# Kernel tuning notes

Hardware: AMD Instinct MI355X
Metric: run time of the kernel (lower is better)

## Reference

```python
import jax, jax.numpy as jnp
import numpy as np

N_NODES = 100000
N_EDGES = 1600000
N_GRAPHS = 512


def setup_inputs() -> dict:
    key = jax.random.key(0)
    k = jax.random.split(key, 6)
    x = jax.random.normal(k[0], (N_NODES, 768), dtype=jnp.float32)
    edge_index = jax.random.randint(k[1], (2, N_EDGES), 0, N_NODES, dtype=jnp.int32)
    batch = jnp.sort(jax.random.randint(k[2], (N_NODES,), 0, N_GRAPHS, dtype=jnp.int32))
    W1 = jax.random.normal(k[3], (768, 256), dtype=jnp.float32) * 0.02
    b1 = jnp.zeros((256,), dtype=jnp.float32)
    W2 = jax.random.normal(k[4], (256, 2), dtype=jnp.float32) * 0.02
    b2 = jnp.zeros((2,), dtype=jnp.float32)
    return {"x": x, "edge_index": edge_index, "batch": batch,
            "W1": W1, "b1": b1, "W2": W2, "b2": b2}


def gcn_conv(x, src, dst, W, b, n_nodes):
    # PyG GCNConv: h = x @ W; add self-loops; symmetric normalization D^-1/2 A D^-1/2
    h = x @ W  # [N, out]
    ones = jnp.ones((src.shape[0],), dtype=x.dtype)
    # degree including self-loop
    deg = jax.ops.segment_sum(ones, dst, num_segments=n_nodes) + 1.0  # [N]
    dinv = jax.lax.rsqrt(deg)
    norm_e = dinv[src] * dinv[dst]  # [E]
    msg = h[src] * norm_e[:, None]  # gather + scale, [E, out]
    agg = jax.ops.segment_sum(msg, dst, num_segments=n_nodes)  # scatter-add
    # self-loop contribution: norm = dinv[i]*dinv[i] = 1/deg[i]
    agg = agg + h * (1.0 / deg)[:, None]
    return agg + b


def reference(x, edge_index, batch, W1, b1, W2, b2):
    n_nodes = x.shape[0]
    src, dst = edge_index[0], edge_index[1]
    h = gcn_conv(x, src, dst, W1, b1, n_nodes)
    h = jax.nn.relu(h)
    # dropout p=0.5 is identity in eval mode (self.training=False)
    h = gcn_conv(h, src, dst, W2, b2, n_nodes)
    # global_mean_pool over batch assignment
    sums = jax.ops.segment_sum(h, batch, num_segments=N_GRAPHS)  # [G, out]
    counts = jax.ops.segment_sum(jnp.ones((n_nodes,), h.dtype), batch, num_segments=N_GRAPHS)
    return sums / jnp.maximum(counts, 1.0)[:, None]
```

## Files before the change

kernel.cpp:

```cpp
#include <hip/hip_runtime.h>

typedef unsigned short u16;
typedef unsigned int   u32;
typedef __bf16 bf16x8 __attribute__((ext_vector_type(8)));
typedef float  f32x4  __attribute__((ext_vector_type(4)));
typedef u32    u32x4  __attribute__((ext_vector_type(4)));
typedef u16    u16x8  __attribute__((ext_vector_type(8)));

#define NF1 768
#define NF2 256

__device__ __forceinline__ u16 f2bf(float f) {
  u32 u = __builtin_bit_cast(u32, f);
  u += 0x7fffu + ((u >> 16) & 1u);
  return (u16)(u >> 16);
}
__device__ __forceinline__ float bf2f(u16 h) {
  return __builtin_bit_cast(float, ((u32)h) << 16);
}

__device__ __forceinline__ void gll16(const void* g, void* l) {
  __builtin_amdgcn_global_load_lds(
      (const __attribute__((address_space(1))) unsigned int*)g,
      (__attribute__((address_space(3))) unsigned int*)l, 16, 0, 0);
}

__global__ void k_zero(u32* __restrict__ p, int n) {
  int i = blockIdx.x * 256 + threadIdx.x;
  if (i < n) p[i] = 0u;
}

__global__ void k_w1t(const float* __restrict__ W1, u16* __restrict__ W1T) {
  int idx = blockIdx.x * 256 + threadIdx.x;
  if (idx < NF1 * NF2) {
    int k = idx >> 8, j = idx & 255;
    W1T[(size_t)j * NF1 + k] = f2bf(W1[idx]);
  }
}

__global__ __launch_bounds__(256) void k_gemm(const float* __restrict__ X,
                                              const u16* __restrict__ W1T,
                                              u16* __restrict__ H1, int M) {
  __shared__ float lsA[128 * 64];
  __shared__ u16   lsB[128 * 64];
  const int t    = threadIdx.x;
  const int m0   = blockIdx.x * 128;
  const int n0   = blockIdx.y * 128;
  const int lane = t & 63;
  const int wid  = t >> 6;
  const int wr   = wid >> 1, wc = wid & 1;

  const int rowbase = wid * 4 + (lane >> 4);
  const int perm_s  = ((rowbase & 7) << 1) | ((rowbase >> 3) & 1);
  const float* srcA[8];
  #pragma unroll
  for (int i = 0; i < 8; ++i) {
    int gr = m0 + i * 16 + rowbase;
    if (gr > M - 1) gr = M - 1;
    srcA[i] = X + (size_t)gr * NF1 + (((lane & 15) ^ perm_s) * 4);
  }
  const int colbase = wid * 8 + (lane >> 3);
  const u16* srcB[4];
  #pragma unroll
  for (int j = 0; j < 4; ++j) {
    int gc = n0 + j * 32 + colbase;
    srcB[j] = W1T + (size_t)gc * NF1 + (((lane & 7) ^ (lane >> 3)) * 8);
  }

  f32x4 acc[4][4];
  #pragma unroll
  for (int m = 0; m < 4; ++m)
    #pragma unroll
    for (int n = 0; n < 4; ++n) { f32x4 z = {0.f, 0.f, 0.f, 0.f}; acc[m][n] = z; }

  const int lm     = lane & 15;
  const int l4     = lane >> 4;
  const int perm_r = ((lane & 7) << 1) | ((lane >> 3) & 1);

  const int NT = NF1 / 64;
  for (int kt = 0; kt < NT; ++kt) {
    #pragma unroll
    for (int i = 0; i < 8; ++i)
      gll16(srcA[i] + kt * 64, &lsA[(i * 16 + wid * 4) * 64]);
    #pragma unroll
    for (int j = 0; j < 4; ++j)
      gll16(srcB[j] + kt * 64, &lsB[(j * 32 + wid * 8) * 64]);
    __syncthreads();

    #pragma unroll
    for (int ks = 0; ks < 2; ++ks) {
      bf16x8 af[4], bfr[4];
      #pragma unroll
      for (int m = 0; m < 4; ++m) {
        int row  = wr * 64 + m * 16 + lm;
        int c    = ks * 4 + l4;
        int ulo  = (2 * c) ^ perm_r;
        const char* base = (const char*)lsA + row * 256;
        float4 L = *(const float4*)(base + ulo * 16);
        float4 H = *(const float4*)(base + (ulo ^ 1) * 16);
        u32 w0, w1, w2, w3;
        asm("v_cvt_pk_bf16_f32 %0, %1, %2" : "=v"(w0) : "v"(L.x), "v"(L.y));
        asm("v_cvt_pk_bf16_f32 %0, %1, %2" : "=v"(w1) : "v"(L.z), "v"(L.w));
        asm("v_cvt_pk_bf16_f32 %0, %1, %2" : "=v"(w2) : "v"(H.x), "v"(H.y));
        asm("v_cvt_pk_bf16_f32 %0, %1, %2" : "=v"(w3) : "v"(H.z), "v"(H.w));
        u32x4 uw = {w0, w1, w2, w3};
        af[m] = __builtin_bit_cast(bf16x8, uw);
      }
      #pragma unroll
      for (int n = 0; n < 4; ++n) {
        int col = wc * 64 + n * 16 + lm;
        int u   = ks * 4 + l4;
        int ph  = u ^ (lane & 7);
        bfr[n] = *(const bf16x8*)((const char*)lsB + col * 128 + ph * 16);
      }
      #pragma unroll
      for (int m = 0; m < 4; ++m)
        #pragma unroll
        for (int n = 0; n < 4; ++n)
          acc[m][n] = __builtin_amdgcn_mfma_f32_16x16x32_bf16(af[m], bfr[n], acc[m][n], 0, 0, 0);
    }
    __syncthreads();
  }

  #pragma unroll
  for (int m = 0; m < 4; ++m) {
    int rowb = m0 + wr * 64 + m * 16 + (lane >> 4) * 4;
    #pragma unroll
    for (int n = 0; n < 4; ++n) {
      int col = n0 + wc * 64 + n * 16 + (lane & 15);
      #pragma unroll
      for (int j = 0; j < 4; ++j) {
        int row = rowb + j;
        if (row < M) H1[(size_t)row * NF2 + col] = f2bf(acc[m][n][j]);
      }
    }
  }
}

__global__ void k_deg(const int* __restrict__ EI, int E, u32* __restrict__ deg) {
  int e = blockIdx.x * 256 + threadIdx.x;
  if (e < E) atomicAdd(&deg[EI[E + e]], 1u);
}

__global__ __launch_bounds__(1024) void k_scan1(const u32* __restrict__ deg,
                                                u32* __restrict__ rowptr,
                                                u32* __restrict__ bsum, int Nn) {
  __shared__ u32 sm[1024];
  int t = threadIdx.x;
  int i = blockIdx.x * 1024 + t;
  u32 v = (i < Nn) ? deg[i] : 0u;
  sm[t] = v;
  __syncthreads();
  #pragma unroll
  for (int off = 1; off < 1024; off <<= 1) {
    u32 x = (t >= off) ? sm[t - off] : 0u;
    __syncthreads();
    sm[t] += x;
    __syncthreads();
  }
  u32 incl = sm[t];
  if (i < Nn) rowptr[i] = incl - v;
  if (t == 1023) bsum[blockIdx.x] = incl;
}

__global__ void k_scan2(const u32* __restrict__ bsum, u32* __restrict__ boff, int nc) {
  __shared__ u32 sm[128];
  int t = threadIdx.x;
  u32 v = (t < nc) ? bsum[t] : 0u;
  sm[t] = v;
  __syncthreads();
  #pragma unroll
  for (int off = 1; off < 128; off <<= 1) {
    u32 x = (t >= off) ? sm[t - off] : 0u;
    __syncthreads();
    sm[t] += x;
    __syncthreads();
  }
  if (t < nc) boff[t] = sm[t] - v;
}

__global__ void k_scan3(u32* __restrict__ rowptr, const u32* __restrict__ boff,
                        u32* __restrict__ cursor, const u32* __restrict__ deg,
                        float* __restrict__ dinv, int Nn, int E) {
  int i = blockIdx.x * 256 + threadIdx.x;
  if (i < Nn) {
    u32 rp = rowptr[i] + boff[i >> 10];
    rowptr[i] = rp;
    cursor[i] = rp;
    dinv[i] = rsqrtf((float)deg[i] + 1.0f);
  }
  if (i == 0) rowptr[Nn] = (u32)E;
}

__global__ void k_fill(const int* __restrict__ EI, int E, int* __restrict__ cursor,
                       int* __restrict__ csr) {
  int e = blockIdx.x * 256 + threadIdx.x;
  if (e < E) {
    int s = EI[e], d = EI[E + e];
    int pos = atomicAdd(&cursor[d], 1);
    csr[pos] = s;
  }
}

__global__ __launch_bounds__(256) void k_agg1(const u16* __restrict__ H1,
                                              const int* __restrict__ csr,
                                              const u32* __restrict__ rowptr,
                                              const float* __restrict__ dinv,
                                              const float* __restrict__ B1,
                                              const float* __restrict__ W2,
                                              float* __restrict__ H2, int Nn) {
  int node = (blockIdx.x << 2) + (threadIdx.x >> 6);
  if (node >= Nn) return;
  const int lane = threadIdx.x & 63;
  const int hl   = lane >> 5;
  const int fo   = (lane & 31) * 8;
  const int rp0 = (int)rowptr[node], rp1 = (int)rowptr[node + 1];
  const float dvi = dinv[node];

  float c0 = 0.f, c1 = 0.f, c2 = 0.f, c3 = 0.f,
        c4 = 0.f, c5 = 0.f, c6 = 0.f, c7 = 0.f;

  for (int e = rp0 + 2 * hl; e < rp1; e += 8) {
    const int eA = e, eB = e + 1, eC = e + 4, eD = e + 5;
    const bool hB = eB < rp1, hC = eC < rp1, hD = eD < rp1;
    const int sA = csr[eA];
    const int sB = hB ? csr[eB] : sA;
    const int sC = hC ? csr[eC] : sA;
    const int sD = hD ? csr[eD] : sA;
    const u16x8 rA = *(const u16x8*)(H1 + (size_t)sA * NF2 + fo);
    const u16x8 rB = *(const u16x8*)(H1 + (size_t)sB * NF2 + fo);
    const u16x8 rC = *(const u16x8*)(H1 + (size_t)sC * NF2 + fo);
    const u16x8 rD = *(const u16x8*)(H1 + (size_t)sD * NF2 + fo);
    const float nA = dinv[sA] * dvi;
    const float nB = hB ? dinv[sB] * dvi : 0.f;
    const float nC = hC ? dinv[sC] * dvi : 0.f;
    const float nD = hD ? dinv[sD] * dvi : 0.f;
    c0 += nA * bf2f(rA[0]) + nB * bf2f(rB[0]) + nC * bf2f(rC[0]) + nD * bf2f(rD[0]);
    c1 += nA * bf2f(rA[1]) + nB * bf2f(rB[1]) + nC * bf2f(rC[1]) + nD * bf2f(rD[1]);
    c2 += nA * bf2f(rA[2]) + nB * bf2f(rB[2]) + nC * bf2f(rC[2]) + nD * bf2f(rD[2]);
    c3 += nA * bf2f(rA[3]) + nB * bf2f(rB[3]) + nC * bf2f(rC[3]) + nD * bf2f(rD[3]);
    c4 += nA * bf2f(rA[4]) + nB * bf2f(rB[4]) + nC * bf2f(rC[4]) + nD * bf2f(rD[4]);
    c5 += nA * bf2f(rA[5]) + nB * bf2f(rB[5]) + nC * bf2f(rC[5]) + nD * bf2f(rD[5]);
    c6 += nA * bf2f(rA[6]) + nB * bf2f(rB[6]) + nC * bf2f(rC[6]) + nD * bf2f(rD[6]);
    c7 += nA * bf2f(rA[7]) + nB * bf2f(rB[7]) + nC * bf2f(rC[7]) + nD * bf2f(rD[7]);
  }

  c0 += __shfl_xor(c0, 32);
  c1 += __shfl_xor(c1, 32);
  c2 += __shfl_xor(c2, 32);
  c3 += __shfl_xor(c3, 32);
  c4 += __shfl_xor(c4, 32);
  c5 += __shfl_xor(c5, 32);
  c6 += __shfl_xor(c6, 32);
  c7 += __shfl_xor(c7, 32);

  {
    const float ns = dvi * dvi;
    const u16x8 rs = *(const u16x8*)(H1 + (size_t)node * NF2 + fo);
    c0 += ns * bf2f(rs[0]); c1 += ns * bf2f(rs[1]);
    c2 += ns * bf2f(rs[2]); c3 += ns * bf2f(rs[3]);
    c4 += ns * bf2f(rs[4]); c5 += ns * bf2f(rs[5]);
    c6 += ns * bf2f(rs[6]); c7 += ns * bf2f(rs[7]);
  }

  const float4 bA = *(const float4*)(B1 + fo);
  const float4 bB = *(const float4*)(B1 + fo + 4);
  const float r0 = fmaxf(c0 + bA.x, 0.f), r1 = fmaxf(c1 + bA.y, 0.f);
  const float r2 = fmaxf(c2 + bA.z, 0.f), r3 = fmaxf(c3 + bA.w, 0.f);
  const float r4 = fmaxf(c4 + bB.x, 0.f), r5 = fmaxf(c5 + bB.y, 0.f);
  const float r6 = fmaxf(c6 + bB.z, 0.f), r7 = fmaxf(c7 + bB.w, 0.f);

  const float4* wp = (const float4*)(W2 + 2 * fo);
  const float4 w0 = wp[0], w1 = wp[1], w2 = wp[2], w3 = wp[3];
  float p0 = r0 * w0.x + r1 * w0.z + r2 * w1.x + r3 * w1.z
           + r4 * w2.x + r5 * w2.z + r6 * w3.x + r7 * w3.z;
  float p1 = r0 * w0.y + r1 * w0.w + r2 * w1.y + r3 * w1.w
           + r4 * w2.y + r5 * w2.w + r6 * w3.y + r7 * w3.w;
  #pragma unroll
  for (int o = 16; o; o >>= 1) {
    p0 += __shfl_xor(p0, o);
    p1 += __shfl_xor(p1, o);
  }
  if (lane == 0) {
    H2[2 * (size_t)node]     = p0;
    H2[2 * (size_t)node + 1] = p1;
  }
}

__global__ __launch_bounds__(256) void k_l2e(const int* __restrict__ EI, int E,
                                             const float* __restrict__ dinv,
                                             const float* __restrict__ H2,
                                             const int* __restrict__ batch,
                                             float* __restrict__ accg) {
  __shared__ float sb[1024];
  for (int i = threadIdx.x; i < 1024; i += 256) sb[i] = 0.f;
  __syncthreads();
  for (int e = blockIdx.x * 256 + threadIdx.x; e < E; e += gridDim.x * 256) {
    int s = EI[e], d = EI[E + e];
    float nrm = dinv[s] * dinv[d];
    float2 hv = *(const float2*)(H2 + 2 * (size_t)s);
    int g = batch[d];
    atomicAdd(&sb[2 * g],     nrm * hv.x);
    atomicAdd(&sb[2 * g + 1], nrm * hv.y);
  }
  __syncthreads();
  for (int i = threadIdx.x; i < 1024; i += 256)
    if (sb[i] != 0.f) atomicAdd(&accg[i], sb[i]);
}

__global__ __launch_bounds__(256) void k_l2n(int Nn, const float* __restrict__ dinv,
                                             const float* __restrict__ H2,
                                             const int* __restrict__ batch,
                                             float* __restrict__ accg,
                                             u32* __restrict__ gcnt) {
  __shared__ float sb[1024];
  __shared__ u32 sc[512];
  for (int i = threadIdx.x; i < 1024; i += 256) sb[i] = 0.f;
  for (int i = threadIdx.x; i < 512; i += 256) sc[i] = 0u;
  __syncthreads();
  for (int i = blockIdx.x * 256 + threadIdx.x; i < Nn; i += gridDim.x * 256) {
    int g = batch[i];
    float dv = dinv[i];
    float ns = dv * dv;
    float2 hv = *(const float2*)(H2 + 2 * (size_t)i);
    atomicAdd(&sb[2 * g],     ns * hv.x);
    atomicAdd(&sb[2 * g + 1], ns * hv.y);
    atomicAdd(&sc[g], 1u);
  }
  __syncthreads();
  for (int i = threadIdx.x; i < 1024; i += 256)
    if (sb[i] != 0.f) atomicAdd(&accg[i], sb[i]);
  for (int i = threadIdx.x; i < 512; i += 256)
    if (sc[i]) atomicAdd(&gcnt[i], sc[i]);
}

__global__ void k_final(const float* __restrict__ accg, const u32* __restrict__ gcnt,
                        const float* __restrict__ B2, float* __restrict__ out) {
  int i = blockIdx.x * 256 + threadIdx.x;
  if (i < 1024) {
    int g = i >> 1, c = i & 1;
    float cnt = (float)gcnt[g];
    float s = accg[i] + cnt * B2[c];
    out[i] = s / fmaxf(cnt, 1.0f);
  }
}

extern "C" void kernel_launch(void* const* d_in, const int* in_sizes, int n_in,
                              void* d_out, int out_size, void* d_ws, size_t ws_size,
                              hipStream_t stream) {
  const float* X     = (const float*)d_in[0];
  const int*   EI    = (const int*)d_in[1];
  const int*   BATCH = (const int*)d_in[2];
  const float* W1    = (const float*)d_in[3];
  const float* B1    = (const float*)d_in[4];
  const float* W2    = (const float*)d_in[5];
  const float* B2    = (const float*)d_in[6];
  const int Nn = in_sizes[0] / NF1;
  const int E  = in_sizes[1] / 2;
  float* OUT = (float*)d_out;
  (void)n_in; (void)out_size; (void)ws_size;

  char* w = (char*)d_ws;
  size_t off = 0;
  auto alloc = [&](size_t bytes) -> void* {
    void* p = w + off;
    off = (off + bytes + 511) & ~(size_t)511;
    return p;
  };
  u32*   deg    = (u32*)alloc((size_t)Nn * 4);
  u32*   rowptr = (u32*)alloc(((size_t)Nn + 1) * 4);
  u32*   cursor = (u32*)alloc((size_t)Nn * 4);
  u32*   bsum   = (u32*)alloc(512);
  u32*   boff   = (u32*)alloc(512);
  float* dinv   = (float*)alloc((size_t)Nn * 4);
  int*   csr    = (int*)alloc((size_t)E * 4);
  u16*   H1     = (u16*)alloc((size_t)Nn * NF2 * 2);
  float* H2     = (float*)alloc((size_t)Nn * 2 * 4);
  float* accg   = (float*)alloc(1536 * 4);
  u32*   gcnt   = (u32*)(accg + 1024);
  u16*   W1T    = (u16*)alloc((size_t)NF1 * NF2 * 2);

  const int NC = (Nn + 1023) >> 10;

  hipLaunchKernelGGL(k_zero, dim3((Nn + 255) / 256), dim3(256), 0, stream, deg, Nn);
  hipLaunchKernelGGL(k_zero, dim3(6), dim3(256), 0, stream, (u32*)accg, 1536);
  hipLaunchKernelGGL(k_w1t, dim3((NF1 * NF2 + 255) / 256), dim3(256), 0, stream, W1, W1T);
  hipLaunchKernelGGL(k_gemm, dim3((Nn + 127) / 128, 2), dim3(256), 0, stream, X, W1T, H1, Nn);
  hipLaunchKernelGGL(k_deg, dim3((E + 255) / 256), dim3(256), 0, stream, EI, E, deg);
  hipLaunchKernelGGL(k_scan1, dim3(NC), dim3(1024), 0, stream, deg, rowptr, bsum, Nn);
  hipLaunchKernelGGL(k_scan2, dim3(1), dim3(128), 0, stream, bsum, boff, NC);
  hipLaunchKernelGGL(k_scan3, dim3((Nn + 255) / 256), dim3(256), 0, stream,
                     rowptr, boff, cursor, deg, dinv, Nn, E);
  hipLaunchKernelGGL(k_fill, dim3((E + 255) / 256), dim3(256), 0, stream,
                     EI, E, (int*)cursor, csr);
  hipLaunchKernelGGL(k_agg1, dim3((Nn + 3) / 4), dim3(256), 0, stream,
                     H1, csr, rowptr, dinv, B1, W2, H2, Nn);
  hipLaunchKernelGGL(k_l2e, dim3(512), dim3(256), 0, stream, EI, E, dinv, H2, BATCH, accg);
  hipLaunchKernelGGL(k_l2n, dim3(256), dim3(256), 0, stream, Nn, dinv, H2, BATCH, accg, gcnt);
  hipLaunchKernelGGL(k_final, dim3(4), dim3(256), 0, stream, accg, gcnt, B2, OUT);
}
```

Baseline: 500.9 us.

## Widen GEMM tile to full 256 columns and double-buffer LDS loads

```diff
diff --git a/kernel.cpp b/kernel.cpp
--- a/kernel.cpp
+++ b/kernel.cpp
@@ -38,14 +38,13 @@
   }
 }
 
-__global__ __launch_bounds__(256) void k_gemm(const float* __restrict__ X,
-                                              const u16* __restrict__ W1T,
-                                              u16* __restrict__ H1, int M) {
-  __shared__ float lsA[128 * 64];
-  __shared__ u16   lsB[128 * 64];
+__global__ __launch_bounds__(256, 1) void k_gemm(const float* __restrict__ X,
+                                                 const u16* __restrict__ W1T,
+                                                 u16* __restrict__ H1, int M) {
+  __shared__ float lsA[2][128 * 64];
+  __shared__ u16   lsB[2][256 * 64];
   const int t    = threadIdx.x;
   const int m0   = blockIdx.x * 128;
-  const int n0   = blockIdx.y * 128;
   const int lane = t & 63;
   const int wid  = t >> 6;
   const int wr   = wid >> 1, wc = wid & 1;
@@ -60,42 +59,55 @@
     srcA[i] = X + (size_t)gr * NF1 + (((lane & 15) ^ perm_s) * 4);
   }
   const int colbase = wid * 8 + (lane >> 3);
-  const u16* srcB[4];
-  #pragma unroll
-  for (int j = 0; j < 4; ++j) {
-    int gc = n0 + j * 32 + colbase;
+  const u16* srcB[8];
+  #pragma unroll
+  for (int j = 0; j < 8; ++j) {
+    int gc = j * 32 + colbase;
     srcB[j] = W1T + (size_t)gc * NF1 + (((lane & 7) ^ (lane >> 3)) * 8);
   }
 
-  f32x4 acc[4][4];
+#define STAGE(kt_, buf_) do {                                                  \
+    _Pragma("unroll")                                                          \
+    for (int i_ = 0; i_ < 8; ++i_)                                             \
+      gll16(srcA[i_] + (kt_) * 64, &lsA[buf_][(i_ * 16 + wid * 4) * 64]);      \
+    _Pragma("unroll")                                                          \
+    for (int j_ = 0; j_ < 8; ++j_)                                             \
+      gll16(srcB[j_] + (kt_) * 64, &lsB[buf_][(j_ * 32 + wid * 8) * 64]);      \
+  } while (0)
+
+  f32x4 acc[4][8];
   #pragma unroll
   for (int m = 0; m < 4; ++m)
     #pragma unroll
-    for (int n = 0; n < 4; ++n) { f32x4 z = {0.f, 0.f, 0.f, 0.f}; acc[m][n] = z; }
+    for (int n = 0; n < 8; ++n) { f32x4 z = {0.f, 0.f, 0.f, 0.f}; acc[m][n] = z; }
 
   const int lm     = lane & 15;
   const int l4     = lane >> 4;
   const int perm_r = ((lane & 7) << 1) | ((lane >> 3) & 1);
 
   const int NT = NF1 / 64;
+  STAGE(0, 0);
+  STAGE(1, 1);
+
+  #pragma unroll
   for (int kt = 0; kt < NT; ++kt) {
-    #pragma unroll
-    for (int i = 0; i < 8; ++i)
-      gll16(srcA[i] + kt * 64, &lsA[(i * 16 + wid * 4) * 64]);
-    #pragma unroll
-    for (int j = 0; j < 4; ++j)
-      gll16(srcB[j] + kt * 64, &lsB[(j * 32 + wid * 8) * 64]);
-    __syncthreads();
-
+    if (kt < NT - 1) { asm volatile("s_waitcnt vmcnt(16)" ::: "memory"); }
+    else             { asm volatile("s_waitcnt vmcnt(0)"  ::: "memory"); }
+    __builtin_amdgcn_sched_barrier(0);
+    asm volatile("s_barrier" ::: "memory");
+    __builtin_amdgcn_sched_barrier(0);
+
+    const float* curA = lsA[kt & 1];
+    const u16*   curB = lsB[kt & 1];
     #pragma unroll
     for (int ks = 0; ks < 2; ++ks) {
-      bf16x8 af[4], bfr[4];
+      bf16x8 af[4], bfr[8];
       #pragma unroll
       for (int m = 0; m < 4; ++m) {
         int row  = wr * 64 + m * 16 + lm;
         int c    = ks * 4 + l4;
         int ulo  = (2 * c) ^ perm_r;
-        const char* base = (const char*)lsA + row * 256;
+        const char* base = (const char*)curA + row * 256;
         float4 L = *(const float4*)(base + ulo * 16);
         float4 H = *(const float4*)(base + (ulo ^ 1) * 16);
         u32 w0, w1, w2, w3;
@@ -107,27 +119,31 @@
         af[m] = __builtin_bit_cast(bf16x8, uw);
       }
       #pragma unroll
-      for (int n = 0; n < 4; ++n) {
-        int col = wc * 64 + n * 16 + lm;
+      for (int n = 0; n < 8; ++n) {
+        int col = wc * 128 + n * 16 + lm;
         int u   = ks * 4 + l4;
         int ph  = u ^ (lane & 7);
-        bfr[n] = *(const bf16x8*)((const char*)lsB + col * 128 + ph * 16);
+        bfr[n] = *(const bf16x8*)((const char*)curB + col * 128 + ph * 16);
       }
       #pragma unroll
       for (int m = 0; m < 4; ++m)
         #pragma unroll
-        for (int n = 0; n < 4; ++n)
+        for (int n = 0; n < 8; ++n)
           acc[m][n] = __builtin_amdgcn_mfma_f32_16x16x32_bf16(af[m], bfr[n], acc[m][n], 0, 0, 0);
     }
-    __syncthreads();
-  }
+
+    __builtin_amdgcn_sched_barrier(0);
+    asm volatile("s_barrier" ::: "memory");
+    if (kt + 2 < NT) STAGE(kt + 2, kt & 1);
+  }
+#undef STAGE
 
   #pragma unroll
   for (int m = 0; m < 4; ++m) {
     int rowb = m0 + wr * 64 + m * 16 + (lane >> 4) * 4;
     #pragma unroll
-    for (int n = 0; n < 4; ++n) {
-      int col = n0 + wc * 64 + n * 16 + (lane & 15);
+    for (int n = 0; n < 8; ++n) {
+      int col = wc * 128 + n * 16 + (lane & 15);
       #pragma unroll
       for (int j = 0; j < 4; ++j) {
         int row = rowb + j;
@@ -385,7 +401,7 @@
   hipLaunchKernelGGL(k_zero, dim3((Nn + 255) / 256), dim3(256), 0, stream, deg, Nn);
   hipLaunchKernelGGL(k_zero, dim3(6), dim3(256), 0, stream, (u32*)accg, 1536);
   hipLaunchKernelGGL(k_w1t, dim3((NF1 * NF2 + 255) / 256), dim3(256), 0, stream, W1, W1T);
-  hipLaunchKernelGGL(k_gemm, dim3((Nn + 127) / 128, 2), dim3(256), 0, stream, X, W1T, H1, Nn);
+  hipLaunchKernelGGL(k_gemm, dim3((Nn + 127) / 128), dim3(256), 0, stream, X, W1T, H1, Nn);
   hipLaunchKernelGGL(k_deg, dim3((E + 255) / 256), dim3(256), 0, stream, EI, E, deg);
   hipLaunchKernelGGL(k_scan1, dim3(NC), dim3(1024), 0, stream, deg, rowptr, bsum, Nn);
   hipLaunchKernelGGL(k_scan2, dim3(1), dim3(128), 0, stream, bsum, boff, NC);
```

Result: faster. 490.3 us (-2.1%).

## Enlarge GEMM tile to 256x256 so X is read once per row block

Applied to the files above, without the earlier changes.

```diff
diff --git a/kernel.cpp b/kernel.cpp
--- a/kernel.cpp
+++ b/kernel.cpp
@@ -38,63 +38,63 @@
   }
 }
 
-__global__ __launch_bounds__(256) void k_gemm(const float* __restrict__ X,
-                                              const u16* __restrict__ W1T,
-                                              u16* __restrict__ H1, int M) {
-  __shared__ float lsA[128 * 64];
-  __shared__ u16   lsB[128 * 64];
+__global__ __launch_bounds__(512, 1) void k_gemm(const float* __restrict__ X,
+                                                 const u16* __restrict__ W1T,
+                                                 u16* __restrict__ H1, int M) {
+  __shared__ float lsA[256 * 64];
+  __shared__ u16   lsB[256 * 64];
   const int t    = threadIdx.x;
-  const int m0   = blockIdx.x * 128;
-  const int n0   = blockIdx.y * 128;
+  const int m0   = blockIdx.x * 256;
   const int lane = t & 63;
   const int wid  = t >> 6;
-  const int wr   = wid >> 1, wc = wid & 1;
-
-  const int rowbase = wid * 4 + (lane >> 4);
-  const int perm_s  = ((rowbase & 7) << 1) | ((rowbase >> 3) & 1);
+  const int wr   = wid >> 1;
+  const int wc   = wid & 1;
+
   const float* srcA[8];
   #pragma unroll
   for (int i = 0; i < 8; ++i) {
-    int gr = m0 + i * 16 + rowbase;
+    int row_l = wid * 32 + i * 4 + (lane >> 4);
+    int perm  = ((row_l & 7) << 1) | ((row_l >> 3) & 1);
+    int gr    = m0 + row_l;
     if (gr > M - 1) gr = M - 1;
-    srcA[i] = X + (size_t)gr * NF1 + (((lane & 15) ^ perm_s) * 4);
-  }
-  const int colbase = wid * 8 + (lane >> 3);
+    srcA[i] = X + (size_t)gr * NF1 + (((lane & 15) ^ perm) * 4);
+  }
   const u16* srcB[4];
   #pragma unroll
   for (int j = 0; j < 4; ++j) {
-    int gc = n0 + j * 32 + colbase;
-    srcB[j] = W1T + (size_t)gc * NF1 + (((lane & 7) ^ (lane >> 3)) * 8);
-  }
-
-  f32x4 acc[4][4];
+    int col_l = wid * 32 + j * 8 + (lane >> 3);
+    srcB[j] = W1T + (size_t)col_l * NF1 + (((lane & 7) ^ (lane >> 3)) * 8);
+  }
+
+  f32x4 acc[4][8];
   #pragma unroll
   for (int m = 0; m < 4; ++m)
     #pragma unroll
-    for (int n = 0; n < 4; ++n) { f32x4 z = {0.f, 0.f, 0.f, 0.f}; acc[m][n] = z; }
+    for (int n = 0; n < 8; ++n) { f32x4 z = {0.f, 0.f, 0.f, 0.f}; acc[m][n] = z; }
 
   const int lm     = lane & 15;
   const int l4     = lane >> 4;
   const int perm_r = ((lane & 7) << 1) | ((lane >> 3) & 1);
+  const int lp     = lane & 7;
 
   const int NT = NF1 / 64;
   for (int kt = 0; kt < NT; ++kt) {
     #pragma unroll
     for (int i = 0; i < 8; ++i)
-      gll16(srcA[i] + kt * 64, &lsA[(i * 16 + wid * 4) * 64]);
+      gll16(srcA[i] + kt * 64, &lsA[(wid * 32 + i * 4) * 64]);
     #pragma unroll
     for (int j = 0; j < 4; ++j)
-      gll16(srcB[j] + kt * 64, &lsB[(j * 32 + wid * 8) * 64]);
+      gll16(srcB[j] + kt * 64, &lsB[(wid * 32 + j * 8) * 64]);
     __syncthreads();
 
     #pragma unroll
     for (int ks = 0; ks < 2; ++ks) {
-      bf16x8 af[4], bfr[4];
+      bf16x8 af[4], bfr[8];
+      const int c = ks * 4 + l4;
       #pragma unroll
       for (int m = 0; m < 4; ++m) {
-        int row  = wr * 64 + m * 16 + lm;
-        int c    = ks * 4 + l4;
-        int ulo  = (2 * c) ^ perm_r;
+        int row = wr * 64 + m * 16 + lm;
+        int ulo = (2 * c) ^ perm_r;
         const char* base = (const char*)lsA + row * 256;
         float4 L = *(const float4*)(base + ulo * 16);
         float4 H = *(const float4*)(base + (ulo ^ 1) * 16);
@@ -107,16 +107,15 @@
         af[m] = __builtin_bit_cast(bf16x8, uw);
       }
       #pragma unroll
-      for (int n = 0; n < 4; ++n) {
-        int col = wc * 64 + n * 16 + lm;
-        int u   = ks * 4 + l4;
-        int ph  = u ^ (lane & 7);
+      for (int n = 0; n < 8; ++n) {
+        int col = wc * 128 + n * 16 + lm;
+        int ph  = c ^ lp;
         bfr[n] = *(const bf16x8*)((const char*)lsB + col * 128 + ph * 16);
       }
       #pragma unroll
       for (int m = 0; m < 4; ++m)
         #pragma unroll
-        for (int n = 0; n < 4; ++n)
+        for (int n = 0; n < 8; ++n)
           acc[m][n] = __builtin_amdgcn_mfma_f32_16x16x32_bf16(af[m], bfr[n], acc[m][n], 0, 0, 0);
     }
     __syncthreads();
@@ -126,8 +125,8 @@
   for (int m = 0; m < 4; ++m) {
     int rowb = m0 + wr * 64 + m * 16 + (lane >> 4) * 4;
     #pragma unroll
-    for (int n = 0; n < 4; ++n) {
-      int col = n0 + wc * 64 + n * 16 + (lane & 15);
+    for (int n = 0; n < 8; ++n) {
+      int col = wc * 128 + n * 16 + (lane & 15);
       #pragma unroll
       for (int j = 0; j < 4; ++j) {
         int row = rowb + j;
@@ -385,7 +384,7 @@
   hipLaunchKernelGGL(k_zero, dim3((Nn + 255) / 256), dim3(256), 0, stream, deg, Nn);
   hipLaunchKernelGGL(k_zero, dim3(6), dim3(256), 0, stream, (u32*)accg, 1536);
   hipLaunchKernelGGL(k_w1t, dim3((NF1 * NF2 + 255) / 256), dim3(256), 0, stream, W1, W1T);
-  hipLaunchKernelGGL(k_gemm, dim3((Nn + 127) / 128, 2), dim3(256), 0, stream, X, W1T, H1, Nn);
+  hipLaunchKernelGGL(k_gemm, dim3((Nn + 255) / 256), dim3(512), 0, stream, X, W1T, H1, Nn);
   hipLaunchKernelGGL(k_deg, dim3((E + 255) / 256), dim3(256), 0, stream, EI, E, deg);
   hipLaunchKernelGGL(k_scan1, dim3(NC), dim3(1024), 0, stream, deg, rowptr, bsum, Nn);
   hipLaunchKernelGGL(k_scan2, dim3(1), dim3(128), 0, stream, bsum, boff, NC);
```

New measurement: 474.8 us. 5.2% less time.
